# Kernel optimization log

Hardware: AMD Instinct MI355X
Metric: run time of the kernel (lower is better)

Reference implementation:

```python
import jax, jax.numpy as jnp
import numpy as np

N_NODES = 50000
N_EDGES = 1600000
IN_DIM = 128
N_HEADS = 8
OUT_DIM = 16
LEAKY_SLOPE = 0.2


def setup_inputs() -> dict:
    key = jax.random.key(0)
    k1, k2, k3, k4, k5, k6 = jax.random.split(key, 6)
    x = jax.random.normal(k1, (N_NODES, IN_DIM), dtype=jnp.float32)
    W = jax.random.normal(k2, (N_HEADS * OUT_DIM, IN_DIM), dtype=jnp.float32) * (1.414 / np.sqrt(IN_DIM))
    attn_l = jax.random.normal(k3, (N_HEADS, OUT_DIM), dtype=jnp.float32) * 0.5
    attn_r = jax.random.normal(k4, (N_HEADS, OUT_DIM), dtype=jnp.float32) * 0.5
    src = jax.random.randint(k5, (N_EDGES,), 0, N_NODES, dtype=jnp.int64) if jax.config.jax_enable_x64 else jax.random.randint(k5, (N_EDGES,), 0, N_NODES, dtype=jnp.int32)
    dst = jax.random.randint(k6, (N_EDGES,), 0, N_NODES, dtype=src.dtype)
    return {"x": x, "W": W, "attn_l": attn_l, "attn_r": attn_r, "src": src, "dst": dst}


def reference(x, W, attn_l, attn_r, src, dst):
    n = x.shape[0]
    # fc projection -> [N, H, D]
    ft = (x @ W.T).reshape(n, N_HEADS, OUT_DIM)
    # per-node attention logits (bmm with [H,D,1] vector == contraction over D) -> [N, H]
    a1 = jnp.einsum('nhd,hd->nh', ft, attn_l)
    a2 = jnp.einsum('nhd,hd->nh', ft, attn_r)
    # per-edge score: leaky_relu(a1[src] + a2[dst]) -> [E, H]
    e = jax.nn.leaky_relu(a1[src] + a2[dst], negative_slope=LEAKY_SLOPE)
    # segment softmax over incoming edges of each dst node (numerically stable)
    seg_max = jax.ops.segment_max(e, dst, num_segments=n)          # [N, H]
    seg_max = jnp.where(jnp.isfinite(seg_max), seg_max, 0.0)       # isolated nodes -> 0
    e_exp = jnp.exp(e - seg_max[dst])                              # [E, H]
    denom = jax.ops.segment_sum(e_exp, dst, num_segments=n)        # [N, H]
    alpha = e_exp / denom[dst]                                     # [E, H]
    # weighted scatter-sum of src messages -> [N, H, D]
    msgs = ft[src] * alpha[:, :, None]                             # [E, H, D]
    out = jax.ops.segment_sum(msgs, dst, num_segments=n)
    return out
```

## Files before the change

kernel.cpp:

```cpp
#include <hip/hip_runtime.h>
#include <math.h>

#define N_NODES 50000
#define N_EDGES 1600000
#define IN_DIM 128
#define N_HEADS 8
#define OUT_DIM 16
#define HD 128
#define NBUCK 784
#define BCAP 2560
#define CHUNK 4096
#define BIN_BLOCKS ((N_EDGES + CHUNK - 1) / CHUNK)
#define NTILE 3125
#define PBLK ((NTILE + 3) / 4)
#define TROW 132
#define LOG2E 1.4426950408889634f

typedef __attribute__((ext_vector_type(8))) short bf16x8;
typedef __attribute__((ext_vector_type(4))) float f32x4;

__device__ __forceinline__ unsigned short f2bf(float f) {
    union { float f; unsigned int u; } v; v.f = f;
    unsigned int u = v.u;
    unsigned int r = (u + 0x7fffu + ((u >> 16) & 1u)) >> 16;
    return (unsigned short)r;
}

__device__ __forceinline__ void scan_nbuck_excl(int* arr, int* part) {
    int t = threadIdx.x;
    int v0 = 0, v1 = 0, v2 = 0, v3 = 0, cs = 0;
    if (t < NBUCK / 4) {
        v0 = arr[4 * t]; v1 = arr[4 * t + 1]; v2 = arr[4 * t + 2]; v3 = arr[4 * t + 3];
        cs = v0 + v1 + v2 + v3;
    }
    part[t] = cs;
    __syncthreads();
    for (int d = 1; d < 256; d <<= 1) {
        int u = (t >= d) ? part[t - d] : 0;
        __syncthreads();
        part[t] += u;
        __syncthreads();
    }
    if (t < NBUCK / 4) {
        int run = part[t] - cs;
        arr[4 * t] = run; run += v0;
        arr[4 * t + 1] = run; run += v1;
        arr[4 * t + 2] = run; run += v2;
        arr[4 * t + 3] = run;
    }
    __syncthreads();
}

__global__ void k_prep(const float* __restrict__ W, unsigned short* __restrict__ Wb,
                       int* __restrict__ bucket_cnt, int* __restrict__ ovf_cnt,
                       unsigned short* __restrict__ ftb, float* __restrict__ a1) {
    int g = blockIdx.x * 256 + threadIdx.x;
    if (g < NBUCK) bucket_cnt[g] = 0;
    if (g == 0) *ovf_cnt = 0;
    if (g < 64) ((unsigned int*)(ftb + (size_t)N_NODES * HD))[g] = 0u;
    if (g >= 64 && g < 64 + N_HEADS)
        a1[(size_t)N_NODES * N_HEADS + (g - 64)] = __int_as_float(0xff800000);
    if (g >= (HD * IN_DIM) / 4) return;
    float4 v = ((const float4*)W)[g];
    ushort4 us;
    us.x = f2bf(v.x); us.y = f2bf(v.y); us.z = f2bf(v.z); us.w = f2bf(v.w);
    ((ushort4*)Wb)[g] = us;
}

__global__ __launch_bounds__(256) void k_proj_bin(
    const float* __restrict__ x, const unsigned short* __restrict__ Wb,
    const float* __restrict__ attn_l, const float* __restrict__ attn_r,
    unsigned short* __restrict__ ftb, float* __restrict__ a1, float* __restrict__ a2,
    const int* __restrict__ src, const int* __restrict__ dst,
    unsigned int* __restrict__ region, int* __restrict__ bucket_cnt,
    int* __restrict__ ovf_cnt, unsigned int* __restrict__ ovf) {
    __shared__ __align__(16) char smem[4 * 16 * TROW * 4];
    int tid = threadIdx.x;

    if (blockIdx.x < PBLK) {
        int wid  = tid >> 6;
        int tile = blockIdx.x * 4 + wid;
        if (tile >= NTILE) return;
        int lane = tid & 63;
        int m = lane & 15, q = lane >> 4;
        int node0 = tile * 16;

        const float* xr = x + (size_t)(node0 + m) * IN_DIM + q * 8;
        float4 xa[4][2];
#pragma unroll
        for (int ks = 0; ks < 4; ks++) {
            xa[ks][0] = *(const float4*)(xr + ks * 32);
            xa[ks][1] = *(const float4*)(xr + ks * 32 + 4);
        }
        bf16x8 afr[4];
#pragma unroll
        for (int ks = 0; ks < 4; ks++) {
            afr[ks][0] = (short)f2bf(xa[ks][0].x); afr[ks][1] = (short)f2bf(xa[ks][0].y);
            afr[ks][2] = (short)f2bf(xa[ks][0].z); afr[ks][3] = (short)f2bf(xa[ks][0].w);
            afr[ks][4] = (short)f2bf(xa[ks][1].x); afr[ks][5] = (short)f2bf(xa[ks][1].y);
            afr[ks][6] = (short)f2bf(xa[ks][1].z); afr[ks][7] = (short)f2bf(xa[ks][1].w);
        }

        float* tl = (float*)smem + wid * (16 * TROW);

#pragma unroll
        for (int h = 0; h < N_HEADS; h++) {
            const unsigned short* wrow = Wb + (size_t)(h * 16 + m) * IN_DIM + q * 8;
            f32x4 c = {0.f, 0.f, 0.f, 0.f};
#pragma unroll
            for (int ks = 0; ks < 4; ks++) {
                bf16x8 bfr = *(const bf16x8*)(wrow + ks * 32);
                c = __builtin_amdgcn_mfma_f32_16x16x32_bf16(afr[ks], bfr, c, 0, 0, 0);
            }
#pragma unroll
            for (int r = 0; r < 4; r++)
                tl[(q * 4 + r) * TROW + h * 16 + m] = c[r];
        }

        int nd = lane & 15;
#pragma unroll
        for (int hi = 0; hi < 2; hi++) {
            int hh = (lane >> 4) + hi * 4;
            const float4* rowv = (const float4*)(tl + nd * TROW + hh * 16);
            const float4* alv  = (const float4*)(attn_l + hh * OUT_DIM);
            const float4* arv  = (const float4*)(attn_r + hh * OUT_DIM);
            float sl = 0.f, sr = 0.f;
#pragma unroll
            for (int d4 = 0; d4 < 4; d4++) {
                float4 fv = rowv[d4];
                float4 al = alv[d4];
                float4 ar = arv[d4];
                sl += fv.x * al.x + fv.y * al.y + fv.z * al.z + fv.w * al.w;
                sr += fv.x * ar.x + fv.y * ar.y + fv.z * ar.z + fv.w * ar.w;
            }
            a1[(node0 + nd) * N_HEADS + hh] = sl * LOG2E;
            a2[(node0 + nd) * N_HEADS + hh] = sr * LOG2E;
        }

#pragma unroll
        for (int p = 0; p < 4; p++) {
            int r = p * 4 + q;
            const float* srcp = tl + r * TROW + m * 8;
            float4 f0 = *(const float4*)(srcp);
            float4 f1 = *(const float4*)(srcp + 4);
            ushort4 u0, u1;
            u0.x = f2bf(f0.x); u0.y = f2bf(f0.y); u0.z = f2bf(f0.z); u0.w = f2bf(f0.w);
            u1.x = f2bf(f1.x); u1.y = f2bf(f1.y); u1.z = f2bf(f1.z); u1.w = f2bf(f1.w);
            ushort4* dstp = (ushort4*)(ftb + (size_t)(node0 + r) * HD + m * 8);
            dstp[0] = u0;
            dstp[1] = u1;
        }
    } else {
        unsigned int* stage = (unsigned int*)smem;
        int* hist  = (int*)(smem + 16384);
        int* delta = (int*)(smem + 19520);
        int* part  = (int*)(smem + 22656);

        int t = tid;
        int base = (blockIdx.x - PBLK) * CHUNK;
        int nvalid = min(CHUNK, N_EDGES - base);

        for (int i = t; i < NBUCK; i += 256) hist[i] = 0;
        __syncthreads();

        unsigned int mypack[CHUNK / 256];
#pragma unroll
        for (int k = 0; k < CHUNK / 256; k++) {
            int i = t + k * 256;
            if (i < nvalid) {
                int s = src[base + i];
                int d = dst[base + i];
                unsigned int p = ((unsigned int)d << 16) | (unsigned int)s;
                mypack[k] = p;
                atomicAdd(&hist[d >> 6], 1);
            }
        }
        __syncthreads();
        for (int i = t; i < NBUCK; i += 256) {
            int h = hist[i];
            delta[i] = (h > 0) ? atomicAdd(&bucket_cnt[i], h) : 0;
        }
        __syncthreads();
        scan_nbuck_excl(hist, part);
        for (int i = t; i < NBUCK; i += 256) delta[i] -= hist[i];
        __syncthreads();
#pragma unroll
        for (int k = 0; k < CHUNK / 256; k++) {
            int i = t + k * 256;
            if (i < nvalid) {
                unsigned int p = mypack[k];
                int slot = atomicAdd(&hist[p >> 22], 1);
                stage[slot] = p;
            }
        }
        __syncthreads();
        for (int i = t; i < nvalid; i += 256) {
            unsigned int p = stage[i];
            int b = p >> 22;
            int pos = delta[b] + i;
            if (pos < BCAP) region[(size_t)b * BCAP + pos] = p;
            else { int o = atomicAdd(ovf_cnt, 1); ovf[o] = p; }
        }
    }
}

__global__ __launch_bounds__(256) void k_place(
    const unsigned int* __restrict__ region, const int* __restrict__ bucket_cnt,
    const int* __restrict__ ovf_cnt, const unsigned int* __restrict__ ovf,
    int* __restrict__ offs, unsigned short* __restrict__ esrc) {
    int b = blockIdx.x;
    int t = threadIdx.x;
    __shared__ int sb[NBUCK], part[256];
    __shared__ int hist[64], sc[64], curs[64];
    __shared__ unsigned short sstage[BCAP];

    for (int i = t; i < NBUCK; i += 256) sb[i] = bucket_cnt[i];
    if (t < 64) hist[t] = 0;
    __syncthreads();
    scan_nbuck_excl(sb, part);

    int truec = bucket_cnt[b];
    int base_b = sb[b];
    int rc = min(truec, BCAP);
    bool fits = (truec <= BCAP);
    const unsigned int* reg = region + (size_t)b * BCAP;

    for (int i = t; i < rc; i += 256) atomicAdd(&hist[(reg[i] >> 16) & 63], 1);
    int no = 0;
    if (truec > BCAP) {
        no = *ovf_cnt;
        for (int i = t; i < no; i += 256)
            if ((int)(ovf[i] >> 22) == b) atomicAdd(&hist[(ovf[i] >> 16) & 63], 1);
    }
    __syncthreads();
    int h = (t < 64) ? hist[t] : 0;
    if (t < 64) sc[t] = h;
    __syncthreads();
    for (int d = 1; d < 64; d <<= 1) {
        int u = (t >= d && t < 64) ? sc[t - d] : 0;
        __syncthreads();
        if (t < 64) sc[t] += u;
        __syncthreads();
    }
    if (t < 64) {
        int pos0 = base_b + sc[t] - h;
        int node = b * 64 + t;
        if (node < N_NODES) offs[node] = pos0;
        curs[t] = pos0;
    }
    if (b == 0 && t == 0) offs[N_NODES] = N_EDGES;
    __syncthreads();
    for (int i = t; i < rc; i += 256) {
        unsigned int p = reg[i];
        int pos = atomicAdd(&curs[(p >> 16) & 63], 1);
        if (fits) sstage[pos - base_b] = (unsigned short)(p & 0xffffu);
        else      esrc[pos] = (unsigned short)(p & 0xffffu);
    }
    if (truec > BCAP) {
        for (int i = t; i < no; i += 256) {
            unsigned int p = ovf[i];
            if ((int)(p >> 22) == b) {
                int pos = atomicAdd(&curs[(p >> 16) & 63], 1);
                esrc[pos] = (unsigned short)(p & 0xffffu);
            }
        }
    }
    __syncthreads();
    if (fits) {
        for (int i = t; i < truec; i += 256)
            esrc[base_b + i] = sstage[i];
    }
}

__device__ __forceinline__ void consume16(const float* a1v, const unsigned int* p,
                                          float a2h, float& l, float& accx, float& accy) {
#pragma unroll
    for (int k = 0; k < 16; k++) {
        float t = a1v[k] + a2h;
        float u = fmaxf(t, 0.2f * t);
        float e;
        asm("v_exp_f32 %0, %1" : "=v"(e) : "v"(u));
        l += e;
        accx = fmaf(e, __uint_as_float(p[k] << 16), accx);
        accy = fmaf(e, __uint_as_float(p[k] & 0xffff0000u), accy);
    }
}

template <int GB>
__device__ __forceinline__ void issue16(int sv, const float* __restrict__ a1,
                                        const unsigned short* __restrict__ ftb,
                                        int hl, int dimoff,
                                        float* a1v, unsigned int* p) {
#pragma unroll
    for (int k = 0; k < 16; k++) {
        int s = __builtin_amdgcn_readlane(sv, GB + k);
        a1v[k] = a1[(size_t)s * N_HEADS + hl];
        p[k]   = *(const unsigned int*)(ftb + (size_t)s * HD + dimoff);
    }
}

__global__ __launch_bounds__(256, 4) void k_aggregate(
    const unsigned short* __restrict__ ftb, const float* __restrict__ a1,
    const float* __restrict__ a2, const int* __restrict__ offs,
    const unsigned short* __restrict__ esrc, float* __restrict__ out) {
    int wid  = threadIdx.x >> 6;
    int lane = threadIdx.x & 63;
    int node = blockIdx.x * 4 + wid;

    int off = __builtin_amdgcn_readfirstlane(offs[node]);
    int deg = __builtin_amdgcn_readfirstlane(offs[node + 1]) - off;
    int hl = lane >> 3;
    float a2h = a2[node * N_HEADS + hl];
    int dimoff = lane * 2;

    const unsigned short* ep = esrc + off;
    float accx = 0.f, accy = 0.f, l = 0.f;

    int done = 0;
    while (done < deg) {
        int nb = deg - done;
        if (nb > 64) nb = 64;
        int v = (int)ep[done + lane];
        int sv = (lane < nb) ? v : N_NODES;

        float a1A[16], a1B[16];
        unsigned int pA[16], pB[16];
        issue16<0>(sv, a1, ftb, hl, dimoff, a1A, pA);
        if (nb > 16) issue16<16>(sv, a1, ftb, hl, dimoff, a1B, pB);
        consume16(a1A, pA, a2h, l, accx, accy);
        if (nb > 32) issue16<32>(sv, a1, ftb, hl, dimoff, a1A, pA);
        if (nb > 16) consume16(a1B, pB, a2h, l, accx, accy);
        if (nb > 48) issue16<48>(sv, a1, ftb, hl, dimoff, a1B, pB);
        if (nb > 32) consume16(a1A, pA, a2h, l, accx, accy);
        if (nb > 48) consume16(a1B, pB, a2h, l, accx, accy);
        done += 64;
    }

    float invl = (deg > 0) ? 1.f / l : 0.f;
    float2 o; o.x = accx * invl; o.y = accy * invl;
    *(float2*)(out + (size_t)node * HD + dimoff) = o;
}

extern "C" void kernel_launch(void* const* d_in, const int* in_sizes, int n_in,
                              void* d_out, int out_size, void* d_ws, size_t ws_size,
                              hipStream_t stream) {
    const float* x      = (const float*)d_in[0];
    const float* W      = (const float*)d_in[1];
    const float* attn_l = (const float*)d_in[2];
    const float* attn_r = (const float*)d_in[3];
    const int*   src    = (const int*)d_in[4];
    const int*   dst    = (const int*)d_in[5];
    float* out = (float*)d_out;

    char* ws = (char*)d_ws;
    size_t o = 0;
    auto alloc = [&](size_t bytes) -> char* {
        char* p = ws + o;
        o = (o + bytes + 255) & ~(size_t)255;
        return p;
    };
    unsigned short* ftb  = (unsigned short*)alloc((size_t)(N_NODES + 1) * HD * 2);
    float* a1            = (float*)alloc((size_t)(N_NODES + 1) * N_HEADS * 4);
    float* a2            = (float*)alloc((size_t)N_NODES * N_HEADS * 4);
    unsigned short* Wb   = (unsigned short*)alloc((size_t)HD * IN_DIM * 2);
    unsigned int* region = (unsigned int*)alloc((size_t)NBUCK * BCAP * 4);
    int* bucket_cnt      = (int*)alloc((size_t)NBUCK * 4);
    int* ovf_cnt         = (int*)alloc(4);
    unsigned int* ovf    = (unsigned int*)alloc((size_t)N_EDGES * 4);
    int* offs            = (int*)alloc((size_t)(N_NODES + 1) * 4);
    unsigned short* esrc = (unsigned short*)alloc((size_t)N_EDGES * 2 + 256);

    (void)in_sizes; (void)n_in; (void)out_size; (void)ws_size;

    k_prep<<<16, 256, 0, stream>>>(W, Wb, bucket_cnt, ovf_cnt, ftb, a1);
    k_proj_bin<<<PBLK + BIN_BLOCKS, 256, 0, stream>>>(
        x, Wb, attn_l, attn_r, ftb, a1, a2,
        src, dst, region, bucket_cnt, ovf_cnt, ovf);
    k_place<<<NBUCK, 256, 0, stream>>>(region, bucket_cnt, ovf_cnt, ovf, offs, esrc);
    k_aggregate<<<N_NODES / 4, 256, 0, stream>>>(ftb, a1, a2, offs, esrc, out);
}
```

Before: 195.1 us.

## Split aggregation into head-pair slices with per-slice a1 layout and edge-group reduction

The aggregation kernel now launches four blocks per group of nodes. Each block handles one slice of two heads (32 feature dims), so a 16-lane group covers one slice and the four groups in a wave each take a quarter of the edges. The partial sums are then combined with cross-lane shuffles. a1 is re-laid out as per-slice interleaved head pairs so each slice gathers from a compact array. This raises parallelism and cuts per-thread register use, at the cost of four times more blocks, repeated loads of offsets and edge lists per slice, and extra shuffle reductions.

After: 223.6 us. +14.6%, slower.

```diff
diff --git a/kernel.cpp b/kernel.cpp
--- a/kernel.cpp
+++ b/kernel.cpp
@@ -53,13 +53,15 @@
 
 __global__ void k_prep(const float* __restrict__ W, unsigned short* __restrict__ Wb,
                        int* __restrict__ bucket_cnt, int* __restrict__ ovf_cnt,
-                       unsigned short* __restrict__ ftb, float* __restrict__ a1) {
+                       unsigned short* __restrict__ ftb, float* __restrict__ a1p) {
     int g = blockIdx.x * 256 + threadIdx.x;
     if (g < NBUCK) bucket_cnt[g] = 0;
     if (g == 0) *ovf_cnt = 0;
     if (g < 64) ((unsigned int*)(ftb + (size_t)N_NODES * HD))[g] = 0u;
-    if (g >= 64 && g < 64 + N_HEADS)
-        a1[(size_t)N_NODES * N_HEADS + (g - 64)] = __int_as_float(0xff800000);
+    if (g >= 64 && g < 72) {
+        int sl = (g - 64) >> 1, pos = (g - 64) & 1;
+        a1p[((size_t)sl * (N_NODES + 1) + N_NODES) * 2 + pos] = __int_as_float(0xff800000);
+    }
     if (g >= (HD * IN_DIM) / 4) return;
     float4 v = ((const float4*)W)[g];
     ushort4 us;
@@ -70,7 +72,7 @@
 __global__ __launch_bounds__(256) void k_proj_bin(
     const float* __restrict__ x, const unsigned short* __restrict__ Wb,
     const float* __restrict__ attn_l, const float* __restrict__ attn_r,
-    unsigned short* __restrict__ ftb, float* __restrict__ a1, float* __restrict__ a2,
+    unsigned short* __restrict__ ftb, float* __restrict__ a1p, float* __restrict__ a2,
     const int* __restrict__ src, const int* __restrict__ dst,
     unsigned int* __restrict__ region, int* __restrict__ bucket_cnt,
     int* __restrict__ ovf_cnt, unsigned int* __restrict__ ovf) {
@@ -133,7 +135,7 @@
                 sl += fv.x * al.x + fv.y * al.y + fv.z * al.z + fv.w * al.w;
                 sr += fv.x * ar.x + fv.y * ar.y + fv.z * ar.z + fv.w * ar.w;
             }
-            a1[(node0 + nd) * N_HEADS + hh] = sl * LOG2E;
+            a1p[((size_t)(hh >> 1) * (N_NODES + 1) + (node0 + nd)) * 2 + (hh & 1)] = sl * LOG2E;
             a2[(node0 + nd) * N_HEADS + hh] = sr * LOG2E;
         }
 
@@ -272,46 +274,49 @@
     }
 }
 
-__device__ __forceinline__ void consume16(const float* a1v, const unsigned int* p,
+__device__ __forceinline__ void stage4s(int sv, int i0, int g,
+    const float* __restrict__ a1p, const unsigned short* __restrict__ ftb,
+    int a1base, int doff, float* a1v, unsigned int* p) {
+#pragma unroll
+    for (int i = 0; i < 4; i++) {
+        int s = __shfl(sv, (i0 + i) * 4 + g);
+        a1v[i] = a1p[a1base + s * 2];
+        p[i]   = *(const unsigned int*)(ftb + (size_t)s * HD + doff);
+    }
+}
+
+__device__ __forceinline__ void consume4s(const float* a1v, const unsigned int* p,
                                           float a2h, float& l, float& accx, float& accy) {
 #pragma unroll
-    for (int k = 0; k < 16; k++) {
-        float t = a1v[k] + a2h;
+    for (int i = 0; i < 4; i++) {
+        float t = a1v[i] + a2h;
         float u = fmaxf(t, 0.2f * t);
         float e;
         asm("v_exp_f32 %0, %1" : "=v"(e) : "v"(u));
         l += e;
-        accx = fmaf(e, __uint_as_float(p[k] << 16), accx);
-        accy = fmaf(e, __uint_as_float(p[k] & 0xffff0000u), accy);
-    }
-}
-
-template <int GB>
-__device__ __forceinline__ void issue16(int sv, const float* __restrict__ a1,
-                                        const unsigned short* __restrict__ ftb,
-                                        int hl, int dimoff,
-                                        float* a1v, unsigned int* p) {
-#pragma unroll
-    for (int k = 0; k < 16; k++) {
-        int s = __builtin_amdgcn_readlane(sv, GB + k);
-        a1v[k] = a1[(size_t)s * N_HEADS + hl];
-        p[k]   = *(const unsigned int*)(ftb + (size_t)s * HD + dimoff);
-    }
-}
-
-__global__ __launch_bounds__(256, 4) void k_aggregate(
-    const unsigned short* __restrict__ ftb, const float* __restrict__ a1,
+        accx = fmaf(e, __uint_as_float(p[i] << 16), accx);
+        accy = fmaf(e, __uint_as_float(p[i] & 0xffff0000u), accy);
+    }
+}
+
+__global__ __launch_bounds__(256) void k_aggregate(
+    const unsigned short* __restrict__ ftb, const float* __restrict__ a1p,
     const float* __restrict__ a2, const int* __restrict__ offs,
     const unsigned short* __restrict__ esrc, float* __restrict__ out) {
     int wid  = threadIdx.x >> 6;
     int lane = threadIdx.x & 63;
-    int node = blockIdx.x * 4 + wid;
+    int slice = blockIdx.x & 3;
+    int node = (blockIdx.x >> 2) * 4 + wid;
+    int g = lane >> 4;
+    int j = lane & 15;
+    int pos = j >> 3;
+    int hl = slice * 2 + pos;
 
     int off = __builtin_amdgcn_readfirstlane(offs[node]);
     int deg = __builtin_amdgcn_readfirstlane(offs[node + 1]) - off;
-    int hl = lane >> 3;
     float a2h = a2[node * N_HEADS + hl];
-    int dimoff = lane * 2;
+    int doff = slice * 32 + j * 2;
+    int a1base = slice * (N_NODES + 1) * 2 + pos;
 
     const unsigned short* ep = esrc + off;
     float accx = 0.f, accy = 0.f, l = 0.f;
@@ -323,22 +328,28 @@
         int v = (int)ep[done + lane];
         int sv = (lane < nb) ? v : N_NODES;
 
-        float a1A[16], a1B[16];
-        unsigned int pA[16], pB[16];
-        issue16<0>(sv, a1, ftb, hl, dimoff, a1A, pA);
-        if (nb > 16) issue16<16>(sv, a1, ftb, hl, dimoff, a1B, pB);
-        consume16(a1A, pA, a2h, l, accx, accy);
-        if (nb > 32) issue16<32>(sv, a1, ftb, hl, dimoff, a1A, pA);
-        if (nb > 16) consume16(a1B, pB, a2h, l, accx, accy);
-        if (nb > 48) issue16<48>(sv, a1, ftb, hl, dimoff, a1B, pB);
-        if (nb > 32) consume16(a1A, pA, a2h, l, accx, accy);
-        if (nb > 48) consume16(a1B, pB, a2h, l, accx, accy);
+        float a1A[4], a1B[4];
+        unsigned int pA[4], pB[4];
+        stage4s(sv, 0, g, a1p, ftb, a1base, doff, a1A, pA);
+        if (nb > 16) stage4s(sv, 4, g, a1p, ftb, a1base, doff, a1B, pB);
+        consume4s(a1A, pA, a2h, l, accx, accy);
+        if (nb > 32) stage4s(sv, 8, g, a1p, ftb, a1base, doff, a1A, pA);
+        if (nb > 16) consume4s(a1B, pB, a2h, l, accx, accy);
+        if (nb > 48) stage4s(sv, 12, g, a1p, ftb, a1base, doff, a1B, pB);
+        if (nb > 32) consume4s(a1A, pA, a2h, l, accx, accy);
+        if (nb > 48) consume4s(a1B, pB, a2h, l, accx, accy);
         done += 64;
     }
 
-    float invl = (deg > 0) ? 1.f / l : 0.f;
-    float2 o; o.x = accx * invl; o.y = accy * invl;
-    *(float2*)(out + (size_t)node * HD + dimoff) = o;
+    accx += __shfl_xor(accx, 16); accx += __shfl_xor(accx, 32);
+    accy += __shfl_xor(accy, 16); accy += __shfl_xor(accy, 32);
+    l    += __shfl_xor(l, 16);    l    += __shfl_xor(l, 32);
+
+    if (g == 0) {
+        float invl = (deg > 0) ? 1.f / l : 0.f;
+        float2 o; o.x = accx * invl; o.y = accy * invl;
+        *(float2*)(out + (size_t)node * HD + doff) = o;
+    }
 }
 
 extern "C" void kernel_launch(void* const* d_in, const int* in_sizes, int n_in,
@@ -360,7 +371,7 @@
         return p;
     };
     unsigned short* ftb  = (unsigned short*)alloc((size_t)(N_NODES + 1) * HD * 2);
-    float* a1            = (float*)alloc((size_t)(N_NODES + 1) * N_HEADS * 4);
+    float* a1p           = (float*)alloc((size_t)4 * (N_NODES + 1) * 2 * 4);
     float* a2            = (float*)alloc((size_t)N_NODES * N_HEADS * 4);
     unsigned short* Wb   = (unsigned short*)alloc((size_t)HD * IN_DIM * 2);
     unsigned int* region = (unsigned int*)alloc((size_t)NBUCK * BCAP * 4);
@@ -372,10 +383,10 @@
 
     (void)in_sizes; (void)n_in; (void)out_size; (void)ws_size;
 
-    k_prep<<<16, 256, 0, stream>>>(W, Wb, bucket_cnt, ovf_cnt, ftb, a1);
+    k_prep<<<16, 256, 0, stream>>>(W, Wb, bucket_cnt, ovf_cnt, ftb, a1p);
     k_proj_bin<<<PBLK + BIN_BLOCKS, 256, 0, stream>>>(
-        x, Wb, attn_l, attn_r, ftb, a1, a2,
+        x, Wb, attn_l, attn_r, ftb, a1p, a2,
         src, dst, region, bucket_cnt, ovf_cnt, ovf);
     k_place<<<NBUCK, 256, 0, stream>>>(region, bucket_cnt, ovf_cnt, ovf, offs, esrc);
-    k_aggregate<<<N_NODES / 4, 256, 0, stream>>>(ftb, a1, a2, offs, esrc, out);
-}
+    k_aggregate<<<N_NODES, 256, 0, stream>>>(ftb, a1p, a2, offs, esrc, out);
+}
```

## Make aggregation persistent with fewer waves and higher occupancy

Applied to the files above, without the earlier changes.

The aggregation kernel now launches a fixed grid of 2048 blocks, and each wave walks a contiguous range of destination nodes instead of handling exactly one node. The double-buffered A/B gather arrays are collapsed into a single 16-wide buffer, which lowers register pressure so launch bounds can rise to 8 blocks per CU. The aim is to cut per-wave launch overhead and raise occupancy to hide gather latency. In exchange it gives up explicit software overlap between gather issue and consume, and contiguous node ranges may leave waves with uneven total degree.

Measured after the change: 206.0 us. 5.6% more time.

```diff
diff --git a/kernel.cpp b/kernel.cpp
--- a/kernel.cpp
+++ b/kernel.cpp
@@ -15,6 +15,8 @@
 #define PBLK ((NTILE + 3) / 4)
 #define TROW 132
 #define LOG2E 1.4426950408889634f
+#define AGG_BLOCKS 2048
+#define AGG_WAVES (AGG_BLOCKS * 4)
 
 typedef __attribute__((ext_vector_type(8))) short bf16x8;
 typedef __attribute__((ext_vector_type(4))) float f32x4;
@@ -299,46 +301,49 @@
     }
 }
 
-__global__ __launch_bounds__(256, 4) void k_aggregate(
+__global__ __launch_bounds__(256, 8) void k_aggregate(
     const unsigned short* __restrict__ ftb, const float* __restrict__ a1,
     const float* __restrict__ a2, const int* __restrict__ offs,
     const unsigned short* __restrict__ esrc, float* __restrict__ out) {
     int wid  = threadIdx.x >> 6;
     int lane = threadIdx.x & 63;
-    int node = blockIdx.x * 4 + wid;
-
-    int off = __builtin_amdgcn_readfirstlane(offs[node]);
-    int deg = __builtin_amdgcn_readfirstlane(offs[node + 1]) - off;
+    int gw = blockIdx.x * 4 + wid;
+    int n0 = __builtin_amdgcn_readfirstlane((int)(((long long)gw * N_NODES) / AGG_WAVES));
+    int n1 = __builtin_amdgcn_readfirstlane((int)(((long long)(gw + 1) * N_NODES) / AGG_WAVES));
     int hl = lane >> 3;
-    float a2h = a2[node * N_HEADS + hl];
     int dimoff = lane * 2;
 
-    const unsigned short* ep = esrc + off;
-    float accx = 0.f, accy = 0.f, l = 0.f;
-
-    int done = 0;
-    while (done < deg) {
-        int nb = deg - done;
-        if (nb > 64) nb = 64;
-        int v = (int)ep[done + lane];
-        int sv = (lane < nb) ? v : N_NODES;
-
-        float a1A[16], a1B[16];
-        unsigned int pA[16], pB[16];
-        issue16<0>(sv, a1, ftb, hl, dimoff, a1A, pA);
-        if (nb > 16) issue16<16>(sv, a1, ftb, hl, dimoff, a1B, pB);
-        consume16(a1A, pA, a2h, l, accx, accy);
-        if (nb > 32) issue16<32>(sv, a1, ftb, hl, dimoff, a1A, pA);
-        if (nb > 16) consume16(a1B, pB, a2h, l, accx, accy);
-        if (nb > 48) issue16<48>(sv, a1, ftb, hl, dimoff, a1B, pB);
-        if (nb > 32) consume16(a1A, pA, a2h, l, accx, accy);
-        if (nb > 48) consume16(a1B, pB, a2h, l, accx, accy);
-        done += 64;
-    }
-
-    float invl = (deg > 0) ? 1.f / l : 0.f;
-    float2 o; o.x = accx * invl; o.y = accy * invl;
-    *(float2*)(out + (size_t)node * HD + dimoff) = o;
+    for (int node = n0; node < n1; ++node) {
+        int off = __builtin_amdgcn_readfirstlane(offs[node]);
+        int deg = __builtin_amdgcn_readfirstlane(offs[node + 1]) - off;
+        float a2h = a2[node * N_HEADS + hl];
+        const unsigned short* ep = esrc + off;
+        float accx = 0.f, accy = 0.f, l = 0.f;
+
+        int done = 0;
+        while (done < deg) {
+            int nb = deg - done;
+            if (nb > 64) nb = 64;
+            int v = (int)ep[done + lane];
+            int sv = (lane < nb) ? v : N_NODES;
+
+            float a1v[16];
+            unsigned int p[16];
+            issue16<0>(sv, a1, ftb, hl, dimoff, a1v, p);
+            consume16(a1v, p, a2h, l, accx, accy);
+            if (nb > 16) { issue16<16>(sv, a1, ftb, hl, dimoff, a1v, p);
+                           consume16(a1v, p, a2h, l, accx, accy); }
+            if (nb > 32) { issue16<32>(sv, a1, ftb, hl, dimoff, a1v, p);
+                           consume16(a1v, p, a2h, l, accx, accy); }
+            if (nb > 48) { issue16<48>(sv, a1, ftb, hl, dimoff, a1v, p);
+                           consume16(a1v, p, a2h, l, accx, accy); }
+            done += 64;
+        }
+
+        float invl = (deg > 0) ? 1.f / l : 0.f;
+        float2 o; o.x = accx * invl; o.y = accy * invl;
+        *(float2*)(out + (size_t)node * HD + dimoff) = o;
+    }
 }
 
 extern "C" void kernel_launch(void* const* d_in, const int* in_sizes, int n_in,
@@ -377,5 +382,5 @@
         x, Wb, attn_l, attn_r, ftb, a1, a2,
         src, dst, region, bucket_cnt, ovf_cnt, ovf);
     k_place<<<NBUCK, 256, 0, stream>>>(region, bucket_cnt, ovf_cnt, ovf, offs, esrc);
-    k_aggregate<<<N_NODES / 4, 256, 0, stream>>>(ftb, a1, a2, offs, esrc, out);
-}
+    k_aggregate<<<AGG_BLOCKS, 256, 0, stream>>>(ftb, a1, a2, offs, esrc, out);
+}
```

## Sort edges into source-range phases and process nodes phase-by-phase for cache locality

Applied to the files above, without the earlier changes.

The place kernel now sorts each destination's edges by source range (7 phases of 8192 nodes) and emits per-node phase offsets. The aggregate kernel becomes persistent, with each wave owning 13 nodes and walking all of its nodes phase by phase. The aim is to keep the gathered ftb and a1 rows for the active source range resident in L2/MALL across concurrent waves. In exchange it loses the 64-edge software-pipelined issue/consume overlap, uses smaller 8-edge batches, and adds a serial per-node loop, which raises latency exposure and register pressure.

Result: slower. 232.2 us (+19.0%).

```diff
diff --git a/kernel.cpp b/kernel.cpp
--- a/kernel.cpp
+++ b/kernel.cpp
@@ -15,6 +15,10 @@
 #define PBLK ((NTILE + 3) / 4)
 #define TROW 132
 #define LOG2E 1.4426950408889634f
+#define NPH 7
+#define AGG_BLOCKS 1024
+#define AGG_WAVES (AGG_BLOCKS * 4)
+#define NPW 13
 
 typedef __attribute__((ext_vector_type(8))) short bf16x8;
 typedef __attribute__((ext_vector_type(4))) float f32x4;
@@ -207,15 +211,15 @@
 __global__ __launch_bounds__(256) void k_place(
     const unsigned int* __restrict__ region, const int* __restrict__ bucket_cnt,
     const int* __restrict__ ovf_cnt, const unsigned int* __restrict__ ovf,
-    int* __restrict__ offs, unsigned short* __restrict__ esrc) {
+    int* __restrict__ nps, unsigned short* __restrict__ esrc) {
     int b = blockIdx.x;
     int t = threadIdx.x;
     __shared__ int sb[NBUCK], part[256];
-    __shared__ int hist[64], sc[64], curs[64];
+    __shared__ int hist[512], sc[512], curs[64 * NPH];
     __shared__ unsigned short sstage[BCAP];
 
     for (int i = t; i < NBUCK; i += 256) sb[i] = bucket_cnt[i];
-    if (t < 64) hist[t] = 0;
+    for (int i = t; i < 512; i += 256) hist[i] = 0;
     __syncthreads();
     scan_nbuck_excl(sb, part);
 
@@ -225,34 +229,55 @@
     bool fits = (truec <= BCAP);
     const unsigned int* reg = region + (size_t)b * BCAP;
 
-    for (int i = t; i < rc; i += 256) atomicAdd(&hist[(reg[i] >> 16) & 63], 1);
+    for (int i = t; i < rc; i += 256) {
+        unsigned int p = reg[i];
+        int key = (int)((p >> 16) & 63) * NPH + (int)((p & 0xffffu) >> 13);
+        atomicAdd(&hist[key], 1);
+    }
     int no = 0;
     if (truec > BCAP) {
         no = *ovf_cnt;
         for (int i = t; i < no; i += 256)
-            if ((int)(ovf[i] >> 22) == b) atomicAdd(&hist[(ovf[i] >> 16) & 63], 1);
-    }
-    __syncthreads();
-    int h = (t < 64) ? hist[t] : 0;
-    if (t < 64) sc[t] = h;
-    __syncthreads();
-    for (int d = 1; d < 64; d <<= 1) {
-        int u = (t >= d && t < 64) ? sc[t - d] : 0;
-        __syncthreads();
-        if (t < 64) sc[t] += u;
-        __syncthreads();
-    }
-    if (t < 64) {
-        int pos0 = base_b + sc[t] - h;
-        int node = b * 64 + t;
-        if (node < N_NODES) offs[node] = pos0;
-        curs[t] = pos0;
-    }
-    if (b == 0 && t == 0) offs[N_NODES] = N_EDGES;
-    __syncthreads();
+            if ((int)(ovf[i] >> 22) == b) {
+                unsigned int p = ovf[i];
+                int key = (int)((p >> 16) & 63) * NPH + (int)((p & 0xffffu) >> 13);
+                atomicAdd(&hist[key], 1);
+            }
+    }
+    __syncthreads();
+
+    {
+        int h0 = hist[2 * t], h1 = hist[2 * t + 1];
+        int ps = h0 + h1;
+        part[t] = ps;
+        __syncthreads();
+        for (int d = 1; d < 256; d <<= 1) {
+            int u = (t >= d) ? part[t - d] : 0;
+            __syncthreads();
+            part[t] += u;
+            __syncthreads();
+        }
+        int run = part[t] - ps;
+        sc[2 * t] = run;
+        sc[2 * t + 1] = run + h0;
+    }
+    __syncthreads();
+
+    for (int i = t; i < 64 * NPH; i += 256) curs[i] = base_b + sc[i];
+    for (int i = t; i < 512; i += 256) {
+        int nl = i >> 3, p = i & 7;
+        int node = b * 64 + nl;
+        if (node < N_NODES) {
+            int v = (p < NPH) ? sc[nl * NPH + p] : sc[(nl + 1) * NPH];
+            nps[node * 8 + p] = base_b + v;
+        }
+    }
+    __syncthreads();
+
     for (int i = t; i < rc; i += 256) {
         unsigned int p = reg[i];
-        int pos = atomicAdd(&curs[(p >> 16) & 63], 1);
+        int key = (int)((p >> 16) & 63) * NPH + (int)((p & 0xffffu) >> 13);
+        int pos = atomicAdd(&curs[key], 1);
         if (fits) sstage[pos - base_b] = (unsigned short)(p & 0xffffu);
         else      esrc[pos] = (unsigned short)(p & 0xffffu);
     }
@@ -260,7 +285,8 @@
         for (int i = t; i < no; i += 256) {
             unsigned int p = ovf[i];
             if ((int)(p >> 22) == b) {
-                int pos = atomicAdd(&curs[(p >> 16) & 63], 1);
+                int key = (int)((p >> 16) & 63) * NPH + (int)((p & 0xffffu) >> 13);
+                int pos = atomicAdd(&curs[key], 1);
                 esrc[pos] = (unsigned short)(p & 0xffffu);
             }
         }
@@ -272,73 +298,72 @@
     }
 }
 
-__device__ __forceinline__ void consume16(const float* a1v, const unsigned int* p,
-                                          float a2h, float& l, float& accx, float& accy) {
-#pragma unroll
-    for (int k = 0; k < 16; k++) {
-        float t = a1v[k] + a2h;
-        float u = fmaxf(t, 0.2f * t);
-        float e;
-        asm("v_exp_f32 %0, %1" : "=v"(e) : "v"(u));
-        l += e;
-        accx = fmaf(e, __uint_as_float(p[k] << 16), accx);
-        accy = fmaf(e, __uint_as_float(p[k] & 0xffff0000u), accy);
-    }
-}
-
-template <int GB>
-__device__ __forceinline__ void issue16(int sv, const float* __restrict__ a1,
-                                        const unsigned short* __restrict__ ftb,
-                                        int hl, int dimoff,
-                                        float* a1v, unsigned int* p) {
-#pragma unroll
-    for (int k = 0; k < 16; k++) {
-        int s = __builtin_amdgcn_readlane(sv, GB + k);
-        a1v[k] = a1[(size_t)s * N_HEADS + hl];
-        p[k]   = *(const unsigned int*)(ftb + (size_t)s * HD + dimoff);
-    }
-}
-
 __global__ __launch_bounds__(256, 4) void k_aggregate(
     const unsigned short* __restrict__ ftb, const float* __restrict__ a1,
-    const float* __restrict__ a2, const int* __restrict__ offs,
+    const float* __restrict__ a2, const int* __restrict__ nps,
     const unsigned short* __restrict__ esrc, float* __restrict__ out) {
     int wid  = threadIdx.x >> 6;
     int lane = threadIdx.x & 63;
-    int node = blockIdx.x * 4 + wid;
-
-    int off = __builtin_amdgcn_readfirstlane(offs[node]);
-    int deg = __builtin_amdgcn_readfirstlane(offs[node + 1]) - off;
+    int gw = blockIdx.x * 4 + wid;
     int hl = lane >> 3;
-    float a2h = a2[node * N_HEADS + hl];
     int dimoff = lane * 2;
 
-    const unsigned short* ep = esrc + off;
-    float accx = 0.f, accy = 0.f, l = 0.f;
-
-    int done = 0;
-    while (done < deg) {
-        int nb = deg - done;
-        if (nb > 64) nb = 64;
-        int v = (int)ep[done + lane];
-        int sv = (lane < nb) ? v : N_NODES;
-
-        float a1A[16], a1B[16];
-        unsigned int pA[16], pB[16];
-        issue16<0>(sv, a1, ftb, hl, dimoff, a1A, pA);
-        if (nb > 16) issue16<16>(sv, a1, ftb, hl, dimoff, a1B, pB);
-        consume16(a1A, pA, a2h, l, accx, accy);
-        if (nb > 32) issue16<32>(sv, a1, ftb, hl, dimoff, a1A, pA);
-        if (nb > 16) consume16(a1B, pB, a2h, l, accx, accy);
-        if (nb > 48) issue16<48>(sv, a1, ftb, hl, dimoff, a1B, pB);
-        if (nb > 32) consume16(a1A, pA, a2h, l, accx, accy);
-        if (nb > 48) consume16(a1B, pB, a2h, l, accx, accy);
-        done += 64;
-    }
-
-    float invl = (deg > 0) ? 1.f / l : 0.f;
-    float2 o; o.x = accx * invl; o.y = accy * invl;
-    *(float2*)(out + (size_t)node * HD + dimoff) = o;
+    int node_l = gw + lane * AGG_WAVES;
+    bool vld = (lane < NPW) && (node_l < N_NODES);
+
+    float accx[NPW], accy[NPW], l[NPW], a2h[NPW];
+#pragma unroll
+    for (int i = 0; i < NPW; i++) {
+        accx[i] = 0.f; accy[i] = 0.f; l[i] = 0.f;
+        int node = gw + i * AGG_WAVES;
+        a2h[i] = (node < N_NODES) ? a2[node * N_HEADS + hl] : 0.f;
+    }
+
+    for (int p = 0; p < NPH; p++) {
+        int stv = vld ? nps[node_l * 8 + p] : 0;
+        int env = vld ? nps[node_l * 8 + p + 1] : 0;
+#pragma unroll
+        for (int i = 0; i < NPW; i++) {
+            int st = __builtin_amdgcn_readlane(stv, i);
+            int en = __builtin_amdgcn_readlane(env, i);
+            for (int base = st; base < en; base += 64) {
+                int nbc = en - base; if (nbc > 64) nbc = 64;
+                int v = (int)esrc[base + lane];
+                int sv = (lane < nbc) ? v : N_NODES;
+                for (int done = 0; done < nbc; done += 8) {
+                    float a1v[8]; unsigned int pv[8];
+#pragma unroll
+                    for (int k = 0; k < 8; k++) {
+                        int s = __builtin_amdgcn_readlane(sv, done + k);
+                        a1v[k] = a1[(size_t)s * N_HEADS + hl];
+                        pv[k]  = *(const unsigned int*)(ftb + (size_t)s * HD + dimoff);
+                    }
+#pragma unroll
+                    for (int k = 0; k < 8; k++) {
+                        float tt = a1v[k] + a2h[i];
+                        float u = fmaxf(tt, 0.2f * tt);
+                        float e;
+                        asm("v_exp_f32 %0, %1" : "=v"(e) : "v"(u));
+                        l[i] += e;
+                        accx[i] = fmaf(e, __uint_as_float(pv[k] << 16), accx[i]);
+                        accy[i] = fmaf(e, __uint_as_float(pv[k] & 0xffff0000u), accy[i]);
+                    }
+                }
+            }
+        }
+    }
+
+    int d0v = vld ? nps[node_l * 8 + 0] : 0;
+    int d7v = vld ? nps[node_l * 8 + 7] : 0;
+#pragma unroll
+    for (int i = 0; i < NPW; i++) {
+        int node = gw + i * AGG_WAVES;
+        if (node >= N_NODES) break;
+        int deg = __builtin_amdgcn_readlane(d7v, i) - __builtin_amdgcn_readlane(d0v, i);
+        float invl = (deg > 0) ? 1.f / l[i] : 0.f;
+        float2 o; o.x = accx[i] * invl; o.y = accy[i] * invl;
+        *(float2*)(out + (size_t)node * HD + dimoff) = o;
+    }
 }
 
 extern "C" void kernel_launch(void* const* d_in, const int* in_sizes, int n_in,
@@ -367,7 +392,7 @@
     int* bucket_cnt      = (int*)alloc((size_t)NBUCK * 4);
     int* ovf_cnt         = (int*)alloc(4);
     unsigned int* ovf    = (unsigned int*)alloc((size_t)N_EDGES * 4);
-    int* offs            = (int*)alloc((size_t)(N_NODES + 1) * 4);
+    int* nps             = (int*)alloc((size_t)N_NODES * 8 * 4);
     unsigned short* esrc = (unsigned short*)alloc((size_t)N_EDGES * 2 + 256);
 
     (void)in_sizes; (void)n_in; (void)out_size; (void)ws_size;
@@ -376,6 +401,6 @@
     k_proj_bin<<<PBLK + BIN_BLOCKS, 256, 0, stream>>>(
         x, Wb, attn_l, attn_r, ftb, a1, a2,
         src, dst, region, bucket_cnt, ovf_cnt, ovf);
-    k_place<<<NBUCK, 256, 0, stream>>>(region, bucket_cnt, ovf_cnt, ovf, offs, esrc);
-    k_aggregate<<<N_NODES / 4, 256, 0, stream>>>(ftb, a1, a2, offs, esrc, out);
-}
+    k_place<<<NBUCK, 256, 0, stream>>>(region, bucket_cnt, ovf_cnt, ovf, nps, esrc);
+    k_aggregate<<<AGG_BLOCKS, 256, 0, stream>>>(ftb, a1, a2, nps, esrc, out);
+}
```
